# Optimization experiments

Measured on AMD Instinct MI355X. Metric: run time of the kernel, lower is better.

## Reference

```python
import jax, jax.numpy as jnp
import numpy as np
import math

B, S, D_MODEL, H = 2, 2048, 1024, 16
HD = D_MODEL // H  # head_dim = 64


def _rope(x, seq_len):
    # x: [B, S, H, HD]; standard rotate-half RoPE with base 10000
    d = x.shape[-1]
    inv_freq = 1.0 / (10000.0 ** (jnp.arange(0, d, 2, dtype=jnp.float32) / d))
    t = jnp.arange(seq_len, dtype=jnp.float32)
    freqs = t[:, None] * inv_freq[None, :]              # [S, HD/2]
    emb = jnp.concatenate([freqs, freqs], axis=-1)      # [S, HD]
    cos = jnp.cos(emb)[None, :, None, :]
    sin = jnp.sin(emb)[None, :, None, :]
    x1, x2 = jnp.split(x, 2, axis=-1)
    rot = jnp.concatenate([-x2, x1], axis=-1)
    return x * cos + rot * sin


def setup_inputs() -> dict:
    key = jax.random.key(0)
    ks = jax.random.split(key, 11)
    s = 1.0 / math.sqrt(D_MODEL)
    return {
        "query": jax.random.normal(ks[0], (B, S, D_MODEL), jnp.float32),
        "keys": jax.random.normal(ks[1], (B, S, D_MODEL), jnp.float32),
        "values": jax.random.normal(ks[2], (B, S, D_MODEL), jnp.float32),
        "Wq": jax.random.normal(ks[3], (D_MODEL, D_MODEL), jnp.float32) * s,
        "bq": jnp.zeros((D_MODEL,), jnp.float32),
        "Wk": jax.random.normal(ks[4], (D_MODEL, D_MODEL), jnp.float32) * s,
        "bk": jnp.zeros((D_MODEL,), jnp.float32),
        "Wv": jax.random.normal(ks[5], (D_MODEL, D_MODEL), jnp.float32) * s,
        "bv": jnp.zeros((D_MODEL,), jnp.float32),
        "Wo": jax.random.normal(ks[6], (D_MODEL, D_MODEL), jnp.float32) * s,
        "bo": jnp.zeros((D_MODEL,), jnp.float32),
    }


def reference(query, keys, values, Wq, bq, Wk, bk, Wv, bv, Wo, bo):
    b, s, _ = query.shape
    scale = math.sqrt(HD)
    q = (query @ Wq.T + bq).reshape(b, s, H, HD)   # [B,S,H,HD]
    k = (keys @ Wk.T + bk).reshape(b, s, H, HD)
    v = (values @ Wv.T + bv).reshape(b, s, H, HD)
    q = _rope(q, s)
    k = _rope(k, s)
    # scores: [B,H,Sq,Sk]
    scores = jnp.einsum('bqhd,bkhd->bhqk', q, k)
    causal = jnp.tril(jnp.ones((s, s), dtype=bool))[None, None]
    scores = jnp.where(causal, scores, -jnp.inf) / scale
    attn = jax.nn.softmax(scores, axis=-1)
    ctx = jnp.einsum('bhqk,bkhd->bqhd', attn, v).reshape(b, s, H * HD)
    out = ctx @ Wo.T + bo
    return out, attn
```

## Files before the change

kernel.cpp:

```cpp
#include <hip/hip_runtime.h>
#include <hip/hip_bf16.h>
#include <stdint.h>
#include <math.h>


typedef __attribute__((ext_vector_type(8))) __bf16 bf16x8;
typedef __attribute__((ext_vector_type(4))) float f32x4;

__device__ __forceinline__ unsigned short f2bf(float f) {
  unsigned int u = __float_as_uint(f);
  u += 0x7fffu + ((u >> 16) & 1u);
  return (unsigned short)(u >> 16);
}

typedef const __attribute__((address_space(1))) unsigned int* gas_ptr;
typedef __attribute__((address_space(3))) unsigned int* las_ptr;
__device__ __forceinline__ void glds16(const void* g, void* l) {
  __builtin_amdgcn_global_load_lds((gas_ptr)g, (las_ptr)l, 16, 0, 0);
}

__global__ __launch_bounds__(256) void rope_table(float2* __restrict__ tab) {
  const int i = blockIdx.x * 256 + threadIdx.x;
  const int spos = i >> 5, d = i & 31;
  const double invf = pow(10000.0, -(double)d / 32.0);
  const double ang = (double)spos * invf;
  double sn, cs;
  sincos(ang, &sn, &cs);
  tab[i] = make_float2((float)cs, (float)sn);
}

__global__ __launch_bounds__(256) void cvt_all(
    const float* __restrict__ a0, const float* __restrict__ a1,
    const float* __restrict__ a2, const float* __restrict__ w0,
    const float* __restrict__ w1, const float* __restrict__ w2,
    const float* __restrict__ w3, unsigned short* __restrict__ ws) {
  const int z = blockIdx.z;
  const float* src;
  unsigned short* dst;
  int n;
  if (z == 0)      { src = a0; dst = ws;             n = 4194304; }
  else if (z == 1) { src = a1; dst = ws + 4194304;   n = 4194304; }
  else if (z == 2) { src = a2; dst = ws + 8388608;   n = 4194304; }
  else if (z == 3) { src = w0; dst = ws + 12582912;  n = 1048576; }
  else if (z == 4) { src = w1; dst = ws + 13631488;  n = 1048576; }
  else if (z == 5) { src = w2; dst = ws + 14680064;  n = 1048576; }
  else             { src = w3; dst = ws + 15728640;  n = 1048576; }
  const int n4 = n >> 2;
  for (int i = blockIdx.x * 256 + threadIdx.x; i < n4; i += gridDim.x * 256) {
    float4 f = ((const float4*)src)[i];
    ushort4 u;
    u.x = f2bf(f.x); u.y = f2bf(f.y); u.z = f2bf(f.z); u.w = f2bf(f.w);
    ((ushort4*)dst)[i] = u;
  }
}

__global__ __launch_bounds__(256) void gemm_qkv(
    const unsigned short* __restrict__ xq, const unsigned short* __restrict__ xk,
    const unsigned short* __restrict__ xv, const unsigned short* __restrict__ wq,
    const unsigned short* __restrict__ wk, const unsigned short* __restrict__ wv,
    const float* __restrict__ bq, const float* __restrict__ bk,
    const float* __restrict__ bv, const float2* __restrict__ rtab,
    unsigned short* __restrict__ qo, unsigned short* __restrict__ ko,
    unsigned short* __restrict__ vo) {
  const int z = blockIdx.z;
  const unsigned short* A = (z == 0) ? xq : (z == 1) ? xk : xv;
  const unsigned short* W = (z == 0) ? wq : (z == 1) ? wk : wv;
  const float* bias = (z == 0) ? bq : (z == 1) ? bk : bv;
  unsigned short* out = (z == 0) ? qo : (z == 1) ? ko : vo;

  const int t = threadIdx.x;
  const int lane = t & 63, wave = t >> 6;
  const int wr = wave >> 1, wc = wave & 1;
  const int lrow = lane & 15, lkb = lane >> 4;
  const int m0 = blockIdx.y * 128, n0 = blockIdx.x * 128;

  __shared__ __align__(16) unsigned short abuf[4096];
  __shared__ __align__(16) unsigned short bbuf[4096];

  f32x4 acc[4][4] = {};

  for (int k0 = 0; k0 < 1024; k0 += 32) {
    __syncthreads();
#pragma unroll
    for (int i = 0; i < 2; ++i) {
      int slot = i * 256 + t;
      int kb = slot >> 7, row = slot & 127;
      glds16(A + (size_t)(m0 + row) * 1024 + k0 + kb * 8, &abuf[slot * 8]);
      glds16(W + (size_t)(n0 + row) * 1024 + k0 + kb * 8, &bbuf[slot * 8]);
    }
    __syncthreads();
    bf16x8 af[4], bfr[4];
#pragma unroll
    for (int mi = 0; mi < 4; ++mi)
      af[mi] = *(const bf16x8*)&abuf[(lkb * 128 + wr * 64 + mi * 16 + lrow) * 8];
#pragma unroll
    for (int ni = 0; ni < 4; ++ni)
      bfr[ni] = *(const bf16x8*)&bbuf[(lkb * 128 + wc * 64 + ni * 16 + lrow) * 8];
#pragma unroll
    for (int mi = 0; mi < 4; ++mi)
#pragma unroll
      for (int ni = 0; ni < 4; ++ni)
        acc[mi][ni] = __builtin_amdgcn_mfma_f32_16x16x32_bf16(af[mi], bfr[ni],
                                                              acc[mi][ni], 0, 0, 0);
  }

  const int nbase = n0 + wc * 64;
  float bias_v[4];
#pragma unroll
  for (int ni = 0; ni < 4; ++ni) bias_v[ni] = bias[nbase + ni * 16 + lrow];

  const int mbase = m0 + wr * 64 + 4 * lkb;
  const bool rope = (z < 2);
  const float qsc = (z == 0) ? 0.125f : 1.0f;

#pragma unroll
  for (int mi = 0; mi < 4; ++mi) {
#pragma unroll
    for (int r = 0; r < 4; ++r) {
      const int m = mbase + mi * 16 + r;
      const int bidx = m >> 11, spos = m & 2047;
      float vals[4];
#pragma unroll
      for (int ni = 0; ni < 4; ++ni) vals[ni] = acc[mi][ni][r] + bias_v[ni];
      if (rope) {
#pragma unroll
        for (int ni = 0; ni < 2; ++ni) {
          const int d = ni * 16 + lrow;
          const float2 cs2 = rtab[spos * 32 + d];
          float x1 = vals[ni], x2 = vals[ni + 2];
          vals[ni] = (x1 * cs2.x - x2 * cs2.y) * qsc;
          vals[ni + 2] = (x2 * cs2.x + x1 * cs2.y) * qsc;
        }
      }
#pragma unroll
      for (int ni = 0; ni < 4; ++ni) {
        const int n = nbase + ni * 16 + lrow;
        const int h = n >> 6, d = n & 63;
        out[(size_t)((bidx * 16 + h) * 2048 + spos) * 64 + d] = f2bf(vals[ni]);
      }
    }
  }
}

__global__ __launch_bounds__(256) void gemm_out(
    const unsigned short* __restrict__ A, const unsigned short* __restrict__ W,
    const float* __restrict__ bias, float* __restrict__ out) {
  const int t = threadIdx.x;
  const int lane = t & 63, wave = t >> 6;
  const int wr = wave >> 1, wc = wave & 1;
  const int lrow = lane & 15, lkb = lane >> 4;
  const int m0 = blockIdx.y * 128, n0 = blockIdx.x * 128;

  __shared__ __align__(16) unsigned short abuf[4096];
  __shared__ __align__(16) unsigned short bbuf[4096];

  f32x4 acc[4][4] = {};

  for (int k0 = 0; k0 < 1024; k0 += 32) {
    __syncthreads();
#pragma unroll
    for (int i = 0; i < 2; ++i) {
      int slot = i * 256 + t;
      int kb = slot >> 7, row = slot & 127;
      glds16(A + (size_t)(m0 + row) * 1024 + k0 + kb * 8, &abuf[slot * 8]);
      glds16(W + (size_t)(n0 + row) * 1024 + k0 + kb * 8, &bbuf[slot * 8]);
    }
    __syncthreads();
    bf16x8 af[4], bfr[4];
#pragma unroll
    for (int mi = 0; mi < 4; ++mi)
      af[mi] = *(const bf16x8*)&abuf[(lkb * 128 + wr * 64 + mi * 16 + lrow) * 8];
#pragma unroll
    for (int ni = 0; ni < 4; ++ni)
      bfr[ni] = *(const bf16x8*)&bbuf[(lkb * 128 + wc * 64 + ni * 16 + lrow) * 8];
#pragma unroll
    for (int mi = 0; mi < 4; ++mi)
#pragma unroll
      for (int ni = 0; ni < 4; ++ni)
        acc[mi][ni] = __builtin_amdgcn_mfma_f32_16x16x32_bf16(af[mi], bfr[ni],
                                                              acc[mi][ni], 0, 0, 0);
  }

  const int nbase = n0 + wc * 64;
  float bias_v[4];
#pragma unroll
  for (int ni = 0; ni < 4; ++ni) bias_v[ni] = bias[nbase + ni * 16 + lrow];
  const int mbase = m0 + wr * 64 + 4 * lkb;
#pragma unroll
  for (int mi = 0; mi < 4; ++mi)
#pragma unroll
    for (int r = 0; r < 4; ++r) {
      const int m = mbase + mi * 16 + r;
      float* orow = out + (size_t)m * 1024 + nbase;
#pragma unroll
      for (int ni = 0; ni < 4; ++ni)
        orow[ni * 16 + lrow] = acc[mi][ni][r] + bias_v[ni];
    }
}

__global__ __launch_bounds__(256) void transpose_v(
    const unsigned short* __restrict__ v, unsigned short* __restrict__ vt) {
  const int s0 = blockIdx.x * 64;
  const int bh = blockIdx.y;
  __shared__ __align__(16) unsigned short tile[64][80];
  const int t = threadIdx.x;
  {
    const int row = t >> 2, cb = t & 3;
    const unsigned short* src = v + (size_t)(bh * 2048 + s0 + row) * 64 + cb * 16;
    *(uint4*)&tile[row][cb * 16] = *(const uint4*)src;
    *(uint4*)&tile[row][cb * 16 + 8] = *(const uint4*)(src + 8);
  }
  __syncthreads();
  {
    const int d = t >> 2, sc = t & 3;
    __align__(16) unsigned short tmp[16];
#pragma unroll
    for (int u = 0; u < 16; ++u) tmp[u] = tile[sc * 16 + u][d];
    unsigned short* dst = vt + (size_t)(bh * 64 + d) * 2048 + s0 + sc * 16;
    *(uint4*)dst = *(const uint4*)&tmp[0];
    *(uint4*)(dst + 8) = *(const uint4*)&tmp[8];
  }
}

__global__ __launch_bounds__(256) void attn_kernel(
    const unsigned short* __restrict__ Q, const unsigned short* __restrict__ Km,
    const unsigned short* __restrict__ Vt, float* __restrict__ attn,
    unsigned short* __restrict__ ctx) {
  const int p = blockIdx.x;
  const int qta = p, qtb = 31 - p;
  const int bh = blockIdx.y;
  const int t = threadIdx.x;
  const int lane = t & 63, wave = t >> 6;
  const int lrow = lane & 15, lg = lane >> 4;
  const int wq0a = qta * 64 + wave * 16;
  const int wq0b = qtb * 64 + wave * 16;

  const unsigned short* Qb = Q + (size_t)bh * 2048 * 64;
  const unsigned short* Kb = Km + (size_t)bh * 2048 * 64;
  const unsigned short* Vb = Vt + (size_t)bh * 64 * 2048;
  float* attn_b = attn + (size_t)bh * 2048 * 2048;

  __shared__ __align__(16) unsigned short kbuf[4096];
  __shared__ __align__(16) unsigned short vbuf[4096];
  __shared__ __align__(16) unsigned short pbuf[4][16 * 68];

  bf16x8 qfa[2], qfb[2];
#pragma unroll
  for (int dk = 0; dk < 2; ++dk) {
    qfa[dk] = *(const bf16x8*)(Qb + (size_t)(wq0a + lrow) * 64 + dk * 32 + lg * 8);
    qfb[dk] = *(const bf16x8*)(Qb + (size_t)(wq0b + lrow) * 64 + dk * 32 + lg * 8);
  }

  float l_a = 0.f, l_b = 0.f;

  auto lupdate = [&](const unsigned short* buf, int kbase, int wq0,
                     const bf16x8* qf, float& l_loc) {
    f32x4 s[4] = {};
#pragma unroll
    for (int fc = 0; fc < 4; ++fc)
#pragma unroll
      for (int dk = 0; dk < 2; ++dk) {
        bf16x8 kf = *(const bf16x8*)&buf[((dk * 4 + lg) * 64 + fc * 16 + lrow) * 8];
        s[fc] = __builtin_amdgcn_mfma_f32_16x16x32_bf16(kf, qf[dk], s[fc], 0, 0, 0);
      }
    const int qg = wq0 + lrow;
    float sum = 0.f;
#pragma unroll
    for (int fc = 0; fc < 4; ++fc)
#pragma unroll
      for (int r = 0; r < 4; ++r) {
        const int kg = kbase + fc * 16 + 4 * lg + r;
        sum += __expf((kg <= qg) ? s[fc][r] : -1e30f);
      }
    l_loc += sum;
  };

  for (int kt = 0; kt <= qtb; kt += 2) {
    const int k0 = kt * 64;
    const bool two = (kt + 1) <= qtb;
    __syncthreads();
#pragma unroll
    for (int i = 0; i < 2; ++i) {
      int slot = i * 256 + t;
      int cb = slot >> 6, row = slot & 63;
      glds16(Kb + (size_t)(k0 + row) * 64 + cb * 8, &kbuf[slot * 8]);
      if (two)
        glds16(Kb + (size_t)(k0 + 64 + row) * 64 + cb * 8, &vbuf[slot * 8]);
    }
    __syncthreads();
    if (kt <= qta) lupdate(kbuf, k0, wq0a, qfa, l_a);
    lupdate(kbuf, k0, wq0b, qfb, l_b);
    if (two) {
      if (kt + 1 <= qta) lupdate(vbuf, k0 + 64, wq0a, qfa, l_a);
      lupdate(vbuf, k0 + 64, wq0b, qfb, l_b);
    }
  }

  l_a += __shfl_xor(l_a, 16); l_a += __shfl_xor(l_a, 32);
  l_b += __shfl_xor(l_b, 16); l_b += __shfl_xor(l_b, 32);
  const float loglinva = -__logf(l_a);
  const float loglinvb = -__logf(l_b);

  f32x4 oaa[4] = {};
  f32x4 oab[4] = {};
  unsigned short* plds = pbuf[wave];

  auto process = [&](int k0, int wq0, const bf16x8* qf, float loglinv,
                     f32x4* oa) {
    f32x4 s[4] = {};
#pragma unroll
    for (int fc = 0; fc < 4; ++fc)
#pragma unroll
      for (int dk = 0; dk < 2; ++dk) {
        bf16x8 kf = *(const bf16x8*)&kbuf[((dk * 4 + lg) * 64 + fc * 16 + lrow) * 8];
        s[fc] = __builtin_amdgcn_mfma_f32_16x16x32_bf16(kf, qf[dk], s[fc], 0, 0, 0);
      }
    const int qg = wq0 + lrow;
    float* arow = attn_b + (size_t)qg * 2048 + k0 + 4 * lg;
#pragma unroll
    for (int fc = 0; fc < 4; ++fc) {
      const int kg0 = k0 + fc * 16 + 4 * lg;
      float4 pv4;
      pv4.x = __expf((kg0 + 0 <= qg) ? s[fc][0] + loglinv : -1e30f);
      pv4.y = __expf((kg0 + 1 <= qg) ? s[fc][1] + loglinv : -1e30f);
      pv4.z = __expf((kg0 + 2 <= qg) ? s[fc][2] + loglinv : -1e30f);
      pv4.w = __expf((kg0 + 3 <= qg) ? s[fc][3] + loglinv : -1e30f);
      *(float4*)(arow + fc * 16) = pv4;
      ushort4 pb;
      pb.x = f2bf(pv4.x); pb.y = f2bf(pv4.y);
      pb.z = f2bf(pv4.z); pb.w = f2bf(pv4.w);
      *(ushort4*)&plds[lrow * 68 + fc * 16 + 4 * lg] = pb;
    }
#pragma unroll
    for (int kk = 0; kk < 2; ++kk) {
      bf16x8 pa = *(const bf16x8*)&plds[lrow * 68 + kk * 32 + lg * 8];
#pragma unroll
      for (int fd = 0; fd < 4; ++fd) {
        bf16x8 vf = *(const bf16x8*)&vbuf[((kk * 4 + lg) * 64 + fd * 16 + lrow) * 8];
        oa[fd] = __builtin_amdgcn_mfma_f32_16x16x32_bf16(pa, vf, oa[fd], 0, 0, 0);
      }
    }
  };

  for (int kt = 0; kt <= qtb; ++kt) {
    const int k0 = kt * 64;
    __syncthreads();
#pragma unroll
    for (int i = 0; i < 2; ++i) {
      int slot = i * 256 + t;
      int cb = slot >> 6, row = slot & 63;
      glds16(Kb + (size_t)(k0 + row) * 64 + cb * 8, &kbuf[slot * 8]);
      glds16(Vb + (size_t)row * 2048 + k0 + cb * 8, &vbuf[slot * 8]);
    }
    __syncthreads();
    if (kt <= qta) process(k0, wq0a, qfa, loglinva, oaa);
    process(k0, wq0b, qfb, loglinvb, oab);
  }

  {
    const int zc0a = (qta + 1) * 16;
    for (int rr = 0; rr < 16; ++rr) {
      float4* arow = (float4*)(attn_b + (size_t)(wq0a + rr) * 2048);
      for (int c = zc0a + lane; c < 512; c += 64)
        arow[c] = make_float4(0.f, 0.f, 0.f, 0.f);
    }
    const int zc0b = (qtb + 1) * 16;
    for (int rr = 0; rr < 16; ++rr) {
      float4* arow = (float4*)(attn_b + (size_t)(wq0b + rr) * 2048);
      for (int c = zc0b + lane; c < 512; c += 64)
        arow[c] = make_float4(0.f, 0.f, 0.f, 0.f);
    }
  }

  const int bidx = bh >> 4, h = bh & 15;
#pragma unroll
  for (int fd = 0; fd < 4; ++fd)
#pragma unroll
    for (int r = 0; r < 4; ++r) {
      const int qga = wq0a + 4 * lg + r;
      const int qgb = wq0b + 4 * lg + r;
      ctx[(size_t)(bidx * 2048 + qga) * 1024 + h * 64 + fd * 16 + lrow] =
          f2bf(oaa[fd][r]);
      ctx[(size_t)(bidx * 2048 + qgb) * 1024 + h * 64 + fd * 16 + lrow] =
          f2bf(oab[fd][r]);
    }
}

extern "C" void kernel_launch(void* const* d_in, const int* in_sizes, int n_in,
                              void* d_out, int out_size, void* d_ws, size_t ws_size,
                              hipStream_t stream) {
  const float* q_in = (const float*)d_in[0];
  const float* k_in = (const float*)d_in[1];
  const float* v_in = (const float*)d_in[2];
  const float* Wq = (const float*)d_in[3];
  const float* bq = (const float*)d_in[4];
  const float* Wk = (const float*)d_in[5];
  const float* bk = (const float*)d_in[6];
  const float* Wv = (const float*)d_in[7];
  const float* bv = (const float*)d_in[8];
  const float* Wo = (const float*)d_in[9];
  const float* bo = (const float*)d_in[10];

  unsigned short* ws = (unsigned short*)d_ws;
  float* outp = (float*)d_out;

  const size_t OXQ = 0, OXK = 4194304, OXV = 8388608;
  const size_t OWQ = 12582912, OWK = 13631488, OWV = 14680064, OWO = 15728640;
  const size_t OQ = 16777216, OK = 20971520, OV = 25165824;
  const size_t OTAB = 29360128;
  const size_t OVT = OXK;
  const size_t OCTX = OXQ;
  float2* rtab = (float2*)(ws + OTAB);

  rope_table<<<dim3(256), 256, 0, stream>>>(rtab);
  cvt_all<<<dim3(512, 1, 7), 256, 0, stream>>>(q_in, k_in, v_in, Wq, Wk, Wv, Wo, ws);
  gemm_qkv<<<dim3(8, 32, 3), 256, 0, stream>>>(ws + OXQ, ws + OXK, ws + OXV,
                                               ws + OWQ, ws + OWK, ws + OWV,
                                               bq, bk, bv, rtab,
                                               ws + OQ, ws + OK, ws + OV);
  transpose_v<<<dim3(32, 32), 256, 0, stream>>>(ws + OV, ws + OVT);
  attn_kernel<<<dim3(16, 32), 256, 0, stream>>>(ws + OQ, ws + OK, ws + OVT,
                                                outp + 4194304, ws + OCTX);
  gemm_out<<<dim3(8, 32), 256, 0, stream>>>(ws + OCTX, ws + OWO, bo, outp);
}
```

Measured before the change: 327.2 us.

## Double-buffer K/V tiles in the attention output pass with async prefetch

The second pass of the attention kernel now keeps two LDS buffers for K and V. It issues global-to-LDS loads for the next tile before computing on the current one, with explicit vmcnt waits and barriers in place of the old two-syncthreads-per-tile pattern. The goal is to hide load latency behind the MFMA, exp and attention-probability store work. In exchange, LDS use roughly doubles, which may lower occupancy, and correctness relies on hand-tuned waitcnt values.

```diff
diff --git a/kernel.cpp b/kernel.cpp
--- a/kernel.cpp
+++ b/kernel.cpp
@@ -240,8 +240,8 @@
   const unsigned short* Vb = Vt + (size_t)bh * 64 * 2048;
   float* attn_b = attn + (size_t)bh * 2048 * 2048;
 
-  __shared__ __align__(16) unsigned short kbuf[4096];
-  __shared__ __align__(16) unsigned short vbuf[4096];
+  __shared__ __align__(16) unsigned short kb[2][4096];
+  __shared__ __align__(16) unsigned short vb[2][4096];
   __shared__ __align__(16) unsigned short pbuf[4][16 * 68];
 
   bf16x8 qfa[2], qfb[2];
@@ -252,6 +252,7 @@
   }
 
   float l_a = 0.f, l_b = 0.f;
+  const int nt = qtb + 1;
 
   auto lupdate = [&](const unsigned short* buf, int kbase, int wq0,
                      const bf16x8* qf, float& l_loc) {
@@ -275,24 +276,24 @@
     l_loc += sum;
   };
 
-  for (int kt = 0; kt <= qtb; kt += 2) {
+  for (int kt = 0; kt < nt; kt += 2) {
     const int k0 = kt * 64;
-    const bool two = (kt + 1) <= qtb;
+    const bool two = (kt + 1) < nt;
     __syncthreads();
 #pragma unroll
     for (int i = 0; i < 2; ++i) {
       int slot = i * 256 + t;
       int cb = slot >> 6, row = slot & 63;
-      glds16(Kb + (size_t)(k0 + row) * 64 + cb * 8, &kbuf[slot * 8]);
+      glds16(Kb + (size_t)(k0 + row) * 64 + cb * 8, &kb[0][slot * 8]);
       if (two)
-        glds16(Kb + (size_t)(k0 + 64 + row) * 64 + cb * 8, &vbuf[slot * 8]);
-    }
-    __syncthreads();
-    if (kt <= qta) lupdate(kbuf, k0, wq0a, qfa, l_a);
-    lupdate(kbuf, k0, wq0b, qfb, l_b);
+        glds16(Kb + (size_t)(k0 + 64 + row) * 64 + cb * 8, &kb[1][slot * 8]);
+    }
+    __syncthreads();
+    if (kt <= qta) lupdate(kb[0], k0, wq0a, qfa, l_a);
+    lupdate(kb[0], k0, wq0b, qfb, l_b);
     if (two) {
-      if (kt + 1 <= qta) lupdate(vbuf, k0 + 64, wq0a, qfa, l_a);
-      lupdate(vbuf, k0 + 64, wq0b, qfb, l_b);
+      if (kt + 1 <= qta) lupdate(kb[1], k0 + 64, wq0a, qfa, l_a);
+      lupdate(kb[1], k0 + 64, wq0b, qfb, l_b);
     }
   }
 
@@ -305,14 +306,25 @@
   f32x4 oab[4] = {};
   unsigned short* plds = pbuf[wave];
 
-  auto process = [&](int k0, int wq0, const bf16x8* qf, float loglinv,
-                     f32x4* oa) {
+  auto stage2 = [&](int kt, int bufi) {
+#pragma unroll
+    for (int i = 0; i < 2; ++i) {
+      int slot = i * 256 + t;
+      int cb = slot >> 6, row = slot & 63;
+      glds16(Kb + (size_t)(kt * 64 + row) * 64 + cb * 8, &kb[bufi][slot * 8]);
+      glds16(Vb + (size_t)row * 2048 + kt * 64 + cb * 8, &vb[bufi][slot * 8]);
+    }
+  };
+
+  auto process2 = [&](int k0, int cur, int wq0, const bf16x8* qf, float loglinv,
+                      f32x4* oa) {
     f32x4 s[4] = {};
 #pragma unroll
     for (int fc = 0; fc < 4; ++fc)
 #pragma unroll
       for (int dk = 0; dk < 2; ++dk) {
-        bf16x8 kf = *(const bf16x8*)&kbuf[((dk * 4 + lg) * 64 + fc * 16 + lrow) * 8];
+        bf16x8 kf =
+            *(const bf16x8*)&kb[cur][((dk * 4 + lg) * 64 + fc * 16 + lrow) * 8];
         s[fc] = __builtin_amdgcn_mfma_f32_16x16x32_bf16(kf, qf[dk], s[fc], 0, 0, 0);
       }
     const int qg = wq0 + lrow;
@@ -336,25 +348,29 @@
       bf16x8 pa = *(const bf16x8*)&plds[lrow * 68 + kk * 32 + lg * 8];
 #pragma unroll
       for (int fd = 0; fd < 4; ++fd) {
-        bf16x8 vf = *(const bf16x8*)&vbuf[((kk * 4 + lg) * 64 + fd * 16 + lrow) * 8];
+        bf16x8 vf =
+            *(const bf16x8*)&vb[cur][((kk * 4 + lg) * 64 + fd * 16 + lrow) * 8];
         oa[fd] = __builtin_amdgcn_mfma_f32_16x16x32_bf16(pa, vf, oa[fd], 0, 0, 0);
       }
     }
   };
 
-  for (int kt = 0; kt <= qtb; ++kt) {
-    const int k0 = kt * 64;
-    __syncthreads();
-#pragma unroll
-    for (int i = 0; i < 2; ++i) {
-      int slot = i * 256 + t;
-      int cb = slot >> 6, row = slot & 63;
-      glds16(Kb + (size_t)(k0 + row) * 64 + cb * 8, &kbuf[slot * 8]);
-      glds16(Vb + (size_t)row * 2048 + k0 + cb * 8, &vbuf[slot * 8]);
-    }
-    __syncthreads();
-    if (kt <= qta) process(k0, wq0a, qfa, loglinva, oaa);
-    process(k0, wq0b, qfb, loglinvb, oab);
+  __syncthreads();
+  stage2(0, 0);
+  __builtin_amdgcn_sched_barrier(0);
+  asm volatile("s_waitcnt vmcnt(0)" ::: "memory");
+  __builtin_amdgcn_s_barrier();
+  __builtin_amdgcn_sched_barrier(0);
+
+  for (int kt = 0; kt < nt; ++kt) {
+    const int cur = kt & 1;
+    if (kt + 1 < nt) stage2(kt + 1, cur ^ 1);
+    if (kt <= qta) process2(kt * 64, cur, wq0a, qfa, loglinva, oaa);
+    process2(kt * 64, cur, wq0b, qfb, loglinvb, oab);
+    __builtin_amdgcn_sched_barrier(0);
+    asm volatile("s_waitcnt vmcnt(4)" ::: "memory");
+    __builtin_amdgcn_s_barrier();
+    __builtin_amdgcn_sched_barrier(0);
   }
 
   {
```

New measurement: 325.6 us. Within noise of the previous version (-0.5%).
